# Kernel tuning notes

Measured on AMD Instinct MI355X. Metric: run time of the kernel, lower is better.

Reference implementation:

```python
import jax, jax.numpy as jnp
import numpy as np


def setup_inputs() -> dict:
    key = jax.random.key(0)
    k1, k2, k3, k4 = jax.random.split(key, 4)
    N, C, T, V = 32, 64, 300, 25
    x = jax.random.normal(k1, (N, C, T, V), dtype=jnp.float32)
    # xavier_uniform-like scale for W (gain=1.414), small normal for alpha/phi
    xavier_scale = 1.414 * (2.0 / (C + C)) ** 0.5
    W = jax.random.normal(k2, (C, C), dtype=jnp.float32) * xavier_scale
    alpha = jax.random.normal(k3, (C // 4, C), dtype=jnp.float32) * 0.1
    phi = jax.random.normal(k4, (C // 4, C), dtype=jnp.float32) * 0.1
    return {"x": x, "W": W, "alpha": alpha, "phi": phi, "kernel": 9, "stride": 2}


def reference(x, W, alpha, phi, kernel, stride):
    N, C, T, V = x.shape
    # [N, C, T, V] -> [N*V, T, C]
    xv = jnp.transpose(x, (0, 3, 2, 1)).reshape(N * V, T, C)
    xw = xv @ W  # [NV, T, C]
    x1 = jnp.einsum('hc,ntc->nth', alpha, xw)  # [NV, T, H]
    x2 = jnp.einsum('hc,ntc->nth', phi, xw)    # [NV, T, H]
    scores = jnp.einsum('nth,nsh->nts', x1, x2)  # [NV, T, T]
    # banded local-window mask I: row i keeps cols |i-j| <= kernel//2 (multiplicative,
    # NOT -inf masking -- faithful to the original torch.mul before softmax)
    idx = jnp.arange(T)
    band = (jnp.abs(idx[:, None] - idx[None, :]) <= kernel // 2).astype(xw.dtype)
    masked = scores * band
    # one-hot selection matmul W_sel @ masked == strided row gather at 0, stride, 2*stride, ...
    sel_rows = jnp.arange(0, T, stride)  # length ceil(T/stride)
    sel = masked[:, sel_rows, :]  # [NV, T', T]
    attn = jax.nn.softmax(sel, axis=-1)
    out = jnp.einsum('nts,nsc->ntc', attn, xw)  # [NV, T', C]
    Tp = out.shape[1]
    # [NV, T', C] -> [N, C, T', V]
    return jnp.transpose(out.reshape(N, V, Tp, C), (0, 3, 2, 1))
```

## Files before the change

### kernel.cpp

```cpp
#include <hip/hip_runtime.h>

#define NB 32
#define CC 64
#define TT 300
#define VV 25
#define HH 16
#define TPOUT 150
#define KH 4
#define TC 4
#define TPG 5

#define ALD 72
#define FLD 100

typedef __attribute__((ext_vector_type(4))) float f32x4;
typedef __attribute__((ext_vector_type(8))) short bf16x8;

static __device__ __forceinline__ unsigned short f2bf(float f) {
    unsigned u = __float_as_uint(f);
    unsigned r = (u + 0x7FFFu + ((u >> 16) & 1u)) >> 16;
    return (unsigned short)r;
}
static __device__ __forceinline__ float bf2f(unsigned short h) {
    return __uint_as_float(((unsigned)h) << 16);
}
static __device__ __forceinline__ float bfLO(unsigned u) {
    return __uint_as_float(u << 16);
}
static __device__ __forceinline__ float bfHI(unsigned u) {
    return __uint_as_float(u & 0xffff0000u);
}

__global__ __launch_bounds__(256) void k0_prep(const float* __restrict__ W,
                                               const float* __restrict__ alpha,
                                               const float* __restrict__ phi,
                                               unsigned short* __restrict__ Wh,
                                               unsigned short* __restrict__ Wl,
                                               float* __restrict__ ssum) {
    const int tid = threadIdx.x;
    {
        int i = blockIdx.x * 256 + tid;
        if (i < 12800)
            reinterpret_cast<float4*>(ssum)[i] = (float4){0.f, 0.f, 0.f, 0.f};
    }
    if (blockIdx.x != 0) return;

    __shared__ float sW[64][64];
    __shared__ float sA[32][64];
    __shared__ float sWe[64][96];
    for (int i = tid; i < 1024; i += 256)
        reinterpret_cast<float4*>(&sW[0][0])[i] = reinterpret_cast<const float4*>(W)[i];
    for (int i = tid; i < 512; i += 256) {
        float4 v = (i < 256) ? reinterpret_cast<const float4*>(alpha)[i]
                             : reinterpret_cast<const float4*>(phi)[i - 256];
        reinterpret_cast<float4*>(&sA[0][0])[i] = v;
    }
    __syncthreads();
    for (int i = tid; i < 1024; i += 256) {
        int ci = i >> 4, q = i & 15;
        *reinterpret_cast<float4*>(&sWe[ci][4 * q]) =
            reinterpret_cast<const float4*>(&sW[ci][0])[q];
    }
    for (int i = tid; i < 2048; i += 256) {
        int ci = i >> 5, j = i & 31;
        const float4* a = reinterpret_cast<const float4*>(&sW[ci][0]);
        const float4* b = reinterpret_cast<const float4*>(&sA[j][0]);
        float acc = 0.f;
#pragma unroll
        for (int q = 0; q < 16; ++q) {
            float4 u = a[q], w = b[q];
            acc += u.x * w.x + u.y * w.y + u.z * w.z + u.w * w.w;
        }
        sWe[ci][64 + j] = acc;
    }
    __syncthreads();
    for (int i = tid; i < 6144; i += 256) {
        int k = i / 96, c = i - 96 * k;
        float f = sWe[k][c];
        unsigned short h = f2bf(f);
        int off = (((k >> 3) * 96) + c) * 8 + (k & 7);
        Wh[off] = h;
        Wl[off] = f2bf(f - bf2f(h));
    }
}

__global__ __launch_bounds__(512) void k1_mfma(const float* __restrict__ x,
                                               const unsigned short* __restrict__ Bh,
                                               const unsigned short* __restrict__ Bl,
                                               unsigned short* __restrict__ xwv,
                                               float* __restrict__ xws1,
                                               float* __restrict__ xws2,
                                               float* __restrict__ ssum) {
    __shared__ __align__(16) char smem[40000];
    unsigned short (*sAh)[ALD] = reinterpret_cast<unsigned short(*)[ALD]>(smem);
    unsigned short (*sAl)[ALD] = reinterpret_cast<unsigned short(*)[ALD]>(smem + 18432);
    float (*sF)[FLD] = reinterpret_cast<float(*)[FLD]>(smem);

    const int n  = blockIdx.y;
    const int t0 = blockIdx.x * TC;
    const int tid = threadIdx.x;

    if (tid < 400) {
        const int cig = tid & 15, tq = tid >> 4;
        const float* xp = x + (size_t)n * CC * TT * VV + (size_t)t0 * VV + 4 * tq;
        unsigned short mh[4][4], ml[4][4];
#pragma unroll
        for (int u = 0; u < 4; ++u) {
            const int ci = cig * 4 + u;
            float4 v = *reinterpret_cast<const float4*>(&xp[(size_t)ci * TT * VV]);
            unsigned short h0 = f2bf(v.x), h1 = f2bf(v.y), h2 = f2bf(v.z), h3 = f2bf(v.w);
            mh[0][u] = h0; mh[1][u] = h1; mh[2][u] = h2; mh[3][u] = h3;
            ml[0][u] = f2bf(v.x - bf2f(h0));
            ml[1][u] = f2bf(v.y - bf2f(h1));
            ml[2][u] = f2bf(v.z - bf2f(h2));
            ml[3][u] = f2bf(v.w - bf2f(h3));
        }
#pragma unroll
        for (int i = 0; i < 4; ++i) {
            *reinterpret_cast<uint2*>(&sAh[4 * tq + i][cig * 4]) =
                *reinterpret_cast<const uint2*>(&mh[i][0]);
            *reinterpret_cast<uint2*>(&sAl[4 * tq + i][cig * 4]) =
                *reinterpret_cast<const uint2*>(&ml[i][0]);
        }
    }
    __syncthreads();

    const int w    = tid >> 6;
    const int lane = tid & 63;
    const int lm   = lane & 15;
    const int g    = lane >> 4;
    const int mc   = w * 16 + lm;

    f32x4 acc[6];
#pragma unroll
    for (int b = 0; b < 6; ++b) acc[b] = (f32x4){0.f, 0.f, 0.f, 0.f};

#pragma unroll
    for (int kh = 0; kh < 2; ++kh) {
        const int kb = kh * 32 + g * 8;
        const int kc = kb >> 3;
        bf16x8 ah = *reinterpret_cast<const bf16x8*>(&sAh[mc][kb]);
        bf16x8 al = *reinterpret_cast<const bf16x8*>(&sAl[mc][kb]);
#pragma unroll
        for (int nt = 0; nt < 6; ++nt) {
            const int nc = nt * 16 + lm;
            bf16x8 bh = *reinterpret_cast<const bf16x8*>(&Bh[(size_t)(kc * 96 + nc) * 8]);
            acc[nt] = __builtin_amdgcn_mfma_f32_16x16x32_bf16(ah, bh, acc[nt], 0, 0, 0);
            if (nt >= 4) {
                bf16x8 bl = *reinterpret_cast<const bf16x8*>(&Bl[(size_t)(kc * 96 + nc) * 8]);
                acc[nt] = __builtin_amdgcn_mfma_f32_16x16x32_bf16(ah, bl, acc[nt], 0, 0, 0);
                acc[nt] = __builtin_amdgcn_mfma_f32_16x16x32_bf16(al, bh, acc[nt], 0, 0, 0);
            }
        }
    }
    __syncthreads();

#pragma unroll
    for (int j = 0; j < 4; ++j) {
        const int row = w * 16 + g * 4 + j;
        if (row < 100) {
#pragma unroll
            for (int nt = 0; nt < 6; ++nt)
                sF[row][nt * 16 + lm] = acc[nt][j];
        }
    }
    __syncthreads();

    for (int i = tid; i < 1600; i += 512) {
        const int vv = i >> 6, c = i & 63;
        float s = sF[vv][c] + sF[vv + 25][c] + sF[vv + 50][c] + sF[vv + 75][c];
        atomicAdd(&ssum[((size_t)n * VV + vv) * CC + c], s);
    }
    for (int i = tid; i < 1600; i += 512) {
        const int row = i >> 4, q = i & 15;
        const int tloc = row / 25, vv = row - 25 * tloc;
        size_t dst = (((size_t)n * VV + vv) * TT + (t0 + tloc)) * CC + 4 * q;
        float4 v = *reinterpret_cast<const float4*>(&sF[row][4 * q]);
        ushort4 b = {f2bf(v.x), f2bf(v.y), f2bf(v.z), f2bf(v.w)};
        *reinterpret_cast<ushort4*>(&xwv[dst]) = b;
    }
    if (tid < 400) {
        const int row = tid >> 2, q = tid & 3;
        const int tloc = row / 25, vv = row - 25 * tloc;
        size_t dst = (((size_t)n * VV + vv) * TT + (t0 + tloc)) * 16 + 4 * q;
        *reinterpret_cast<float4*>(&xws2[dst]) =
            *reinterpret_cast<const float4*>(&sF[row][80 + 4 * q]);
    }
    if (tid < 200) {
        const int re = tid >> 2, q = tid & 3;
        const int te = re / 25, vv = re - 25 * te;
        const int tp = (t0 + 2 * te) >> 1;
        size_t dst = (((size_t)n * VV + vv) * TPOUT + tp) * 16 + 4 * q;
        *reinterpret_cast<float4*>(&xws1[dst]) =
            *reinterpret_cast<const float4*>(&sF[2 * te * 25 + vv][64 + 4 * q]);
    }
}

__global__ __launch_bounds__(512) void k2_fused(const unsigned short* __restrict__ xwv,
                                                const float* __restrict__ xws1,
                                                const float* __restrict__ xws2,
                                                const float* __restrict__ ssum,
                                                float* __restrict__ out) {
    const int tpg = blockIdx.x;
    const int n   = blockIdx.y;
    const int tid = threadIdx.x;
    const int tp0 = tpg * TPG;

    __shared__ unsigned short sOut[TPG * VV][66];
    __shared__ float sss[VV][CC];
    __shared__ float sscore[TPG][VV][9];
    __shared__ float scoef[TPG][VV][10];

    for (int i = tid; i < VV * CC; i += 512)
        (&sss[0][0])[i] = ssum[((size_t)n * VV) * CC + i];

    for (int j = tid; j < TPG * VV * 9; j += 512) {
        const int tpl = j / (VV * 9);
        const int rem = j - tpl * (VV * 9);
        const int v = rem / 9, k = rem - 9 * v;
        const int t = 2 * (tp0 + tpl);
        const int s = t - KH + k;
        float sc = 0.f;
        if (s >= 0 && s < TT) {
            const size_t r = (size_t)n * VV + v;
            const float4* x1 = reinterpret_cast<const float4*>(&xws1[(r * TPOUT + tp0 + tpl) * 16]);
            const float4* x2 = reinterpret_cast<const float4*>(&xws2[(r * TT + s) * 16]);
#pragma unroll
            for (int q = 0; q < 4; ++q) {
                float4 a = x1[q], b = x2[q];
                sc += a.x * b.x + a.y * b.y + a.z * b.z + a.w * b.w;
            }
        }
        sscore[tpl][v][k] = sc;
    }
    __syncthreads();

    for (int j = tid; j < TPG * VV; j += 512) {
        const int tpl = j / VV, v = j - tpl * VV;
        const int t = 2 * (tp0 + tpl);
        float m = 0.f;
        int nb = 0;
#pragma unroll
        for (int k = 0; k < 9; ++k) {
            int s = t - KH + k;
            if (s >= 0 && s < TT) { nb++; m = fmaxf(m, sscore[tpl][v][k]); }
        }
        float wbg = __expf(-m);
        float Z = (float)(TT - nb) * wbg;
        float e[9];
#pragma unroll
        for (int k = 0; k < 9; ++k) {
            int s = t - KH + k;
            float ek = (s >= 0 && s < TT) ? __expf(sscore[tpl][v][k] - m) : 0.f;
            e[k] = ek;
            Z += ek;
        }
        float inv = 1.f / Z;
#pragma unroll
        for (int k = 0; k < 9; ++k) {
            int s = t - KH + k;
            scoef[tpl][v][k] = (s >= 0 && s < TT) ? (e[k] - wbg) * inv : 0.f;
        }
        scoef[tpl][v][9] = wbg * inv;
    }
    __syncthreads();

    for (int j = tid; j < TPG * VV * 8; j += 512) {
        const int w  = j >> 3;
        const int cg = j & 7;
        const int tpl = w / VV, v = w - tpl * VV;
        const int t = 2 * (tp0 + tpl);
        const size_t rbase = ((size_t)n * VV + v) * TT;
        const int c0 = cg * 8;

        float val[8];
        {
            const float cbg = scoef[tpl][v][9];
#pragma unroll
            for (int i = 0; i < 8; ++i) val[i] = cbg * sss[v][c0 + i];
        }
#pragma unroll
        for (int k = 0; k < 9; ++k) {
            int s = t - KH + k;
            s = min(max(s, 0), TT - 1);
            const float cf = scoef[tpl][v][k];
            uint4 u = *reinterpret_cast<const uint4*>(&xwv[(rbase + s) * CC + c0]);
            val[0] = fmaf(cf, bfLO(u.x), val[0]);
            val[1] = fmaf(cf, bfHI(u.x), val[1]);
            val[2] = fmaf(cf, bfLO(u.y), val[2]);
            val[3] = fmaf(cf, bfHI(u.y), val[3]);
            val[4] = fmaf(cf, bfLO(u.z), val[4]);
            val[5] = fmaf(cf, bfHI(u.z), val[5]);
            val[6] = fmaf(cf, bfLO(u.w), val[6]);
            val[7] = fmaf(cf, bfHI(u.w), val[7]);
        }
#pragma unroll
        for (int i = 0; i < 8; ++i) sOut[w][c0 + i] = f2bf(val[i]);
    }
    __syncthreads();

    float* dst = out + ((size_t)n * CC * TPOUT * VV + (size_t)tp0 * VV);
    for (int j = tid; j < CC * TPG * VV; j += 512) {
        const int c = j / (TPG * VV);
        const int w = j - c * (TPG * VV);
        dst[(size_t)c * (TPOUT * VV) + w] = bf2f(sOut[w][c]);
    }
}

extern "C" void kernel_launch(void* const* d_in, const int* in_sizes, int n_in,
                              void* d_out, int out_size, void* d_ws, size_t ws_size,
                              hipStream_t stream) {
    const float* x     = (const float*)d_in[0];
    const float* W     = (const float*)d_in[1];
    const float* alpha = (const float*)d_in[2];
    const float* phi   = (const float*)d_in[3];
    float* out = (float*)d_out;

    float* xws2 = (float*)d_ws;
    float* xws1 = xws2 + (size_t)800 * 300 * 16;
    float* ssum = xws1 + (size_t)800 * 150 * 16;
    unsigned short* xwv = (unsigned short*)(ssum + (size_t)800 * 64);
    unsigned short* Wh  = xwv + (size_t)800 * 300 * CC;
    unsigned short* Wl  = Wh + 6144;

    k0_prep<<<64, 256, 0, stream>>>(W, alpha, phi, Wh, Wl, ssum);
    dim3 g1(TT / TC, NB);
    k1_mfma<<<g1, 512, 0, stream>>>(x, Wh, Wl, xwv, xws1, xws2, ssum);
    dim3 g2(TPOUT / TPG, NB);
    k2_fused<<<g2, 512, 0, stream>>>(xwv, xws1, xws2, ssum, out);
}
```

Measured before the change: 68.70 us.

## Process three time tiles per k1 block and overlap next loads with epilogue

Each k1 block now loops over three consecutive time tiles instead of one, cutting the grid by three. The global loads of x for the next tile are issued before the previous tile's epilogue (atomic sums and bf16/fp32 stores) runs, so load latency can hide behind the epilogue stores. The trade-off is fewer blocks (800 instead of 2400), which lowers parallelism and occupancy, and the extra registers that hold the loaded tile while the epilogue runs.

```diff
diff --git a/kernel.cpp b/kernel.cpp
--- a/kernel.cpp
+++ b/kernel.cpp
@@ -8,6 +8,7 @@
 #define TPOUT 150
 #define KH 4
 #define TC 4
+#define TPB 3
 #define TPG 5
 
 #define ALD 72
@@ -84,6 +85,38 @@
     }
 }
 
+#define K1_EPILOGUE(P0)                                                          \
+    {                                                                            \
+        for (int i = tid; i < 1600; i += 512) {                                  \
+            const int vv = i >> 6, c = i & 63;                                   \
+            float s = sF[vv][c] + sF[vv + 25][c] + sF[vv + 50][c] + sF[vv + 75][c]; \
+            atomicAdd(&ssum[((size_t)n * VV + vv) * CC + c], s);                 \
+        }                                                                        \
+        for (int i = tid; i < 1600; i += 512) {                                  \
+            const int row = i >> 4, q = i & 15;                                  \
+            const int tloc = row / 25, vv = row - 25 * tloc;                     \
+            size_t dst = (((size_t)n * VV + vv) * TT + ((P0) + tloc)) * CC + 4 * q; \
+            float4 v = *reinterpret_cast<const float4*>(&sF[row][4 * q]);        \
+            ushort4 b = {f2bf(v.x), f2bf(v.y), f2bf(v.z), f2bf(v.w)};            \
+            *reinterpret_cast<ushort4*>(&xwv[dst]) = b;                          \
+        }                                                                        \
+        if (tid < 400) {                                                         \
+            const int row = tid >> 2, q = tid & 3;                               \
+            const int tloc = row / 25, vv = row - 25 * tloc;                     \
+            size_t dst = (((size_t)n * VV + vv) * TT + ((P0) + tloc)) * 16 + 4 * q; \
+            *reinterpret_cast<float4*>(&xws2[dst]) =                             \
+                *reinterpret_cast<const float4*>(&sF[row][80 + 4 * q]);          \
+        }                                                                        \
+        if (tid < 200) {                                                         \
+            const int re = tid >> 2, q = tid & 3;                                \
+            const int te = re / 25, vv = re - 25 * te;                           \
+            const int tp = ((P0) + 2 * te) >> 1;                                 \
+            size_t dst = (((size_t)n * VV + vv) * TPOUT + tp) * 16 + 4 * q;      \
+            *reinterpret_cast<float4*>(&xws1[dst]) =                             \
+                *reinterpret_cast<const float4*>(&sF[2 * te * 25 + vv][64 + 4 * q]); \
+        }                                                                        \
+    }
+
 __global__ __launch_bounds__(512) void k1_mfma(const float* __restrict__ x,
                                                const unsigned short* __restrict__ Bh,
                                                const unsigned short* __restrict__ Bl,
@@ -97,102 +130,95 @@
     float (*sF)[FLD] = reinterpret_cast<float(*)[FLD]>(smem);
 
     const int n  = blockIdx.y;
-    const int t0 = blockIdx.x * TC;
+    const int tg = blockIdx.x;
     const int tid = threadIdx.x;
-
-    if (tid < 400) {
-        const int cig = tid & 15, tq = tid >> 4;
-        const float* xp = x + (size_t)n * CC * TT * VV + (size_t)t0 * VV + 4 * tq;
-        unsigned short mh[4][4], ml[4][4];
-#pragma unroll
-        for (int u = 0; u < 4; ++u) {
-            const int ci = cig * 4 + u;
-            float4 v = *reinterpret_cast<const float4*>(&xp[(size_t)ci * TT * VV]);
-            unsigned short h0 = f2bf(v.x), h1 = f2bf(v.y), h2 = f2bf(v.z), h3 = f2bf(v.w);
-            mh[0][u] = h0; mh[1][u] = h1; mh[2][u] = h2; mh[3][u] = h3;
-            ml[0][u] = f2bf(v.x - bf2f(h0));
-            ml[1][u] = f2bf(v.y - bf2f(h1));
-            ml[2][u] = f2bf(v.z - bf2f(h2));
-            ml[3][u] = f2bf(v.w - bf2f(h3));
-        }
-#pragma unroll
-        for (int i = 0; i < 4; ++i) {
-            *reinterpret_cast<uint2*>(&sAh[4 * tq + i][cig * 4]) =
-                *reinterpret_cast<const uint2*>(&mh[i][0]);
-            *reinterpret_cast<uint2*>(&sAl[4 * tq + i][cig * 4]) =
-                *reinterpret_cast<const uint2*>(&ml[i][0]);
-        }
-    }
-    __syncthreads();
-
     const int w    = tid >> 6;
     const int lane = tid & 63;
     const int lm   = lane & 15;
     const int g    = lane >> 4;
     const int mc   = w * 16 + lm;
-
-    f32x4 acc[6];
-#pragma unroll
-    for (int b = 0; b < 6; ++b) acc[b] = (f32x4){0.f, 0.f, 0.f, 0.f};
-
-#pragma unroll
-    for (int kh = 0; kh < 2; ++kh) {
-        const int kb = kh * 32 + g * 8;
-        const int kc = kb >> 3;
-        bf16x8 ah = *reinterpret_cast<const bf16x8*>(&sAh[mc][kb]);
-        bf16x8 al = *reinterpret_cast<const bf16x8*>(&sAl[mc][kb]);
-#pragma unroll
-        for (int nt = 0; nt < 6; ++nt) {
-            const int nc = nt * 16 + lm;
-            bf16x8 bh = *reinterpret_cast<const bf16x8*>(&Bh[(size_t)(kc * 96 + nc) * 8]);
-            acc[nt] = __builtin_amdgcn_mfma_f32_16x16x32_bf16(ah, bh, acc[nt], 0, 0, 0);
-            if (nt >= 4) {
-                bf16x8 bl = *reinterpret_cast<const bf16x8*>(&Bl[(size_t)(kc * 96 + nc) * 8]);
-                acc[nt] = __builtin_amdgcn_mfma_f32_16x16x32_bf16(ah, bl, acc[nt], 0, 0, 0);
-                acc[nt] = __builtin_amdgcn_mfma_f32_16x16x32_bf16(al, bh, acc[nt], 0, 0, 0);
-            }
-        }
-    }
-    __syncthreads();
-
-#pragma unroll
-    for (int j = 0; j < 4; ++j) {
-        const int row = w * 16 + g * 4 + j;
-        if (row < 100) {
-#pragma unroll
-            for (int nt = 0; nt < 6; ++nt)
-                sF[row][nt * 16 + lm] = acc[nt][j];
-        }
-    }
-    __syncthreads();
-
-    for (int i = tid; i < 1600; i += 512) {
-        const int vv = i >> 6, c = i & 63;
-        float s = sF[vv][c] + sF[vv + 25][c] + sF[vv + 50][c] + sF[vv + 75][c];
-        atomicAdd(&ssum[((size_t)n * VV + vv) * CC + c], s);
-    }
-    for (int i = tid; i < 1600; i += 512) {
-        const int row = i >> 4, q = i & 15;
-        const int tloc = row / 25, vv = row - 25 * tloc;
-        size_t dst = (((size_t)n * VV + vv) * TT + (t0 + tloc)) * CC + 4 * q;
-        float4 v = *reinterpret_cast<const float4*>(&sF[row][4 * q]);
-        ushort4 b = {f2bf(v.x), f2bf(v.y), f2bf(v.z), f2bf(v.w)};
-        *reinterpret_cast<ushort4*>(&xwv[dst]) = b;
-    }
-    if (tid < 400) {
-        const int row = tid >> 2, q = tid & 3;
-        const int tloc = row / 25, vv = row - 25 * tloc;
-        size_t dst = (((size_t)n * VV + vv) * TT + (t0 + tloc)) * 16 + 4 * q;
-        *reinterpret_cast<float4*>(&xws2[dst]) =
-            *reinterpret_cast<const float4*>(&sF[row][80 + 4 * q]);
-    }
-    if (tid < 200) {
-        const int re = tid >> 2, q = tid & 3;
-        const int te = re / 25, vv = re - 25 * te;
-        const int tp = (t0 + 2 * te) >> 1;
-        size_t dst = (((size_t)n * VV + vv) * TPOUT + tp) * 16 + 4 * q;
-        *reinterpret_cast<float4*>(&xws1[dst]) =
-            *reinterpret_cast<const float4*>(&sF[2 * te * 25 + vv][64 + 4 * q]);
+    const int cig  = tid & 15, tq = tid >> 4;
+
+#pragma unroll
+    for (int it = 0; it < TPB; ++it) {
+        const int t0 = (tg * TPB + it) * TC;
+
+        float4 ld0, ld1, ld2, ld3;
+        if (tid < 400) {
+            const float* xp = x + (size_t)n * CC * TT * VV + (size_t)t0 * VV + 4 * tq;
+            ld0 = *reinterpret_cast<const float4*>(&xp[(size_t)(cig * 4 + 0) * TT * VV]);
+            ld1 = *reinterpret_cast<const float4*>(&xp[(size_t)(cig * 4 + 1) * TT * VV]);
+            ld2 = *reinterpret_cast<const float4*>(&xp[(size_t)(cig * 4 + 2) * TT * VV]);
+            ld3 = *reinterpret_cast<const float4*>(&xp[(size_t)(cig * 4 + 3) * TT * VV]);
+        }
+
+        if (it > 0) {
+            const int p0 = (tg * TPB + it - 1) * TC;
+            K1_EPILOGUE(p0);
+        }
+        __syncthreads();
+
+        if (tid < 400) {
+            unsigned short mh[4][4], ml[4][4];
+            float4 lds4[4] = {ld0, ld1, ld2, ld3};
+#pragma unroll
+            for (int u = 0; u < 4; ++u) {
+                float4 v = lds4[u];
+                unsigned short h0 = f2bf(v.x), h1 = f2bf(v.y), h2 = f2bf(v.z), h3 = f2bf(v.w);
+                mh[0][u] = h0; mh[1][u] = h1; mh[2][u] = h2; mh[3][u] = h3;
+                ml[0][u] = f2bf(v.x - bf2f(h0));
+                ml[1][u] = f2bf(v.y - bf2f(h1));
+                ml[2][u] = f2bf(v.z - bf2f(h2));
+                ml[3][u] = f2bf(v.w - bf2f(h3));
+            }
+#pragma unroll
+            for (int i = 0; i < 4; ++i) {
+                *reinterpret_cast<uint2*>(&sAh[4 * tq + i][cig * 4]) =
+                    *reinterpret_cast<const uint2*>(&mh[i][0]);
+                *reinterpret_cast<uint2*>(&sAl[4 * tq + i][cig * 4]) =
+                    *reinterpret_cast<const uint2*>(&ml[i][0]);
+            }
+        }
+        __syncthreads();
+
+        f32x4 acc[6];
+#pragma unroll
+        for (int b = 0; b < 6; ++b) acc[b] = (f32x4){0.f, 0.f, 0.f, 0.f};
+#pragma unroll
+        for (int kh = 0; kh < 2; ++kh) {
+            const int kb = kh * 32 + g * 8;
+            const int kc = kb >> 3;
+            bf16x8 ah = *reinterpret_cast<const bf16x8*>(&sAh[mc][kb]);
+            bf16x8 al = *reinterpret_cast<const bf16x8*>(&sAl[mc][kb]);
+#pragma unroll
+            for (int nt = 0; nt < 6; ++nt) {
+                const int nc = nt * 16 + lm;
+                bf16x8 bh = *reinterpret_cast<const bf16x8*>(&Bh[(size_t)(kc * 96 + nc) * 8]);
+                acc[nt] = __builtin_amdgcn_mfma_f32_16x16x32_bf16(ah, bh, acc[nt], 0, 0, 0);
+                if (nt >= 4) {
+                    bf16x8 bl = *reinterpret_cast<const bf16x8*>(&Bl[(size_t)(kc * 96 + nc) * 8]);
+                    acc[nt] = __builtin_amdgcn_mfma_f32_16x16x32_bf16(ah, bl, acc[nt], 0, 0, 0);
+                    acc[nt] = __builtin_amdgcn_mfma_f32_16x16x32_bf16(al, bh, acc[nt], 0, 0, 0);
+                }
+            }
+        }
+        __syncthreads();
+
+#pragma unroll
+        for (int j = 0; j < 4; ++j) {
+            const int row = w * 16 + g * 4 + j;
+            if (row < 100) {
+#pragma unroll
+                for (int nt = 0; nt < 6; ++nt)
+                    sF[row][nt * 16 + lm] = acc[nt][j];
+            }
+        }
+        __syncthreads();
+    }
+
+    {
+        const int p0 = (tg * TPB + TPB - 1) * TC;
+        K1_EPILOGUE(p0);
     }
 }
 
@@ -324,7 +350,7 @@
     unsigned short* Wl  = Wh + 6144;
 
     k0_prep<<<64, 256, 0, stream>>>(W, alpha, phi, Wh, Wl, ssum);
-    dim3 g1(TT / TC, NB);
+    dim3 g1(TT / (TC * TPB), NB);
     k1_mfma<<<g1, 512, 0, stream>>>(x, Wh, Wl, xwv, xws1, xws2, ssum);
     dim3 g2(TPOUT / TPG, NB);
     k2_fused<<<g2, 512, 0, stream>>>(xwv, xws1, xws2, ssum, out);
```

Result: slower. 80.34 us (+16.9%).
